# Kernel tuning notes

Measured on AMD Instinct MI355X. Metric: run time of the kernel, lower is better.

The kernel has to match this reference:

```python
import jax, jax.numpy as jnp
import numpy as np


def _bilinear2d(uv, table):
    """Bilinear lookup with wrap addressing; sigmoid non-linearity applied per
    corner (normalize=True in SpatialGrid2D), matching training-time forward.
    uv: (N,2) in [0,1); table: (U,V,L). Returns (N,L)."""
    U, V, _ = table.shape
    su = uv[:, 0] * U
    sv = uv[:, 1] * V
    u0 = jnp.floor(su)
    v0 = jnp.floor(sv)
    fu = (su - u0)[:, None]  # fractional weights, (N,1)
    fv = (sv - v0)[:, None]
    u0i = jnp.mod(u0.astype(jnp.int32), U)
    v0i = jnp.mod(v0.astype(jnp.int32), V)
    u1i = jnp.mod(u0i + 1, U)
    v1i = jnp.mod(v0i + 1, V)
    t00 = jax.nn.sigmoid(table[u0i, v0i])
    t10 = jax.nn.sigmoid(table[u1i, v0i])
    t01 = jax.nn.sigmoid(table[u0i, v1i])
    t11 = jax.nn.sigmoid(table[u1i, v1i])
    return (t00 * (1 - fu) + t10 * fu) * (1 - fv) + (t01 * (1 - fu) + t11 * fu) * fv


def setup_inputs() -> dict:
    key = jax.random.key(0)
    k1, k2, k3 = jax.random.split(key, 3)
    N = 2048 * 2048  # query points (one per pixel)
    RES = 520        # grid0 resolution from nativeResolution=4096, compression=6
    x = jax.random.uniform(k1, (N, 2), dtype=jnp.float32)
    grid1_table = jax.random.normal(k2, (RES * 4, RES * 4, 2), dtype=jnp.float32)
    grid0_table = jax.random.normal(k3, (RES, RES, 3), dtype=jnp.float32)
    return {"x": x, "grid1_table": grid1_table, "grid0_table": grid0_table}


def reference(x, grid1_table, grid0_table):
    # forward: grid0(grid1(x)) -- chained bilinear indirection lookups
    key = _bilinear2d(x, grid1_table)   # (N,2) indirected uv coords in (0,1)
    return _bilinear2d(key, grid0_table)  # (N,3) decoded RGB
```

## Files before the change

### kernel.cpp

```cpp
#include <hip/hip_runtime.h>
#include <math.h>


typedef float f32x2 __attribute__((ext_vector_type(2)));
typedef float f32x4 __attribute__((ext_vector_type(4)));

__device__ __forceinline__ float mul_rn_nocontract(float a, float b) {
    float r;
    asm("v_mul_f32 %0, %1, %2" : "=v"(r) : "v"(a), "v"(b));
    return r;
}

__device__ __forceinline__ float sigmoid_f64(float t) {
    double e = exp(-(double)t);
    return (float)(1.0 / (1.0 + e));
}

__device__ __forceinline__ float sigmoid_fast(float t) {
    return 1.0f / (1.0f + __expf(-t));
}

__global__ void __launch_bounds__(256) sigmoid_table_kernel(
    const float4* __restrict__ in, float4* __restrict__ out, int n4)
{
    int i = blockIdx.x * blockDim.x + threadIdx.x;
    if (i >= n4) return;
    float4 v = in[i];
    float4 r;
    r.x = sigmoid_f64(v.x);
    r.y = sigmoid_f64(v.y);
    r.z = sigmoid_f64(v.z);
    r.w = sigmoid_f64(v.w);
    out[i] = r;
}

__global__ void __launch_bounds__(256) pack_corners_kernel(
    const float* __restrict__ g1, float* __restrict__ pk, int U1)
{
    int c = blockIdx.x * blockDim.x + threadIdx.x;
    int ncells = U1 * U1;
    if (c >= ncells) return;
    int u = c / U1;
    int v = c - u * U1;
    int u1 = (u + 1 == U1) ? 0 : u + 1;
    int v1 = (v + 1 == U1) ? 0 : v + 1;
    const float2* g = reinterpret_cast<const float2*>(g1);
    float2 a = g[u * U1 + v];
    float2 b = g[u * U1 + v1];
    float2 d = g[u1 * U1 + v];
    float2 e = g[u1 * U1 + v1];
    float4 lo = make_float4(sigmoid_f64(a.x), sigmoid_f64(a.y),
                            sigmoid_f64(b.x), sigmoid_f64(b.y));
    float4 hi = make_float4(sigmoid_f64(d.x), sigmoid_f64(d.y),
                            sigmoid_f64(e.x), sigmoid_f64(e.y));
    float4* o = reinterpret_cast<float4*>(pk + (size_t)c * 8);
    o[0] = lo;
    o[1] = hi;
}

__global__ void __launch_bounds__(256) query_packed_kernel(
    const float* __restrict__ x,
    const float* __restrict__ pk,
    const float* __restrict__ s0,
    float* __restrict__ out,
    int N, int U1, int U0)
{
    int i = blockIdx.x * blockDim.x + threadIdx.x;
    if (i >= N) return;

    f32x2 uv = __builtin_nontemporal_load(
        reinterpret_cast<const f32x2*>(x) + i);

    float fU1 = (float)U1;
    float su = mul_rn_nocontract(uv.x, fU1);
    float sv = mul_rn_nocontract(uv.y, fU1);
    float u0f = floorf(su), v0f = floorf(sv);
    float fu = su - u0f;
    float fv = sv - v0f;
    int u0 = (int)u0f % U1; if (u0 < 0) u0 += U1;
    int v0 = (int)v0f % U1; if (v0 < 0) v0 += U1;

    const float4* cell = reinterpret_cast<const float4*>(pk)
                       + (size_t)(u0 * U1 + v0) * 2;
    float4 lo = cell[0];
    float4 hi = cell[1];

    float omfu = 1.0f - fu, omfv = 1.0f - fv;
    float kx = (lo.x * omfu + hi.x * fu) * omfv
             + (lo.z * omfu + hi.z * fu) * fv;
    float ky = (lo.y * omfu + hi.y * fu) * omfv
             + (lo.w * omfu + hi.w * fu) * fv;

    float fU0 = (float)U0;
    float su2 = mul_rn_nocontract(kx, fU0);
    float sv2 = mul_rn_nocontract(ky, fU0);
    float u0f2 = floorf(su2), v0f2 = floorf(sv2);
    float fu2 = su2 - u0f2, fv2 = sv2 - v0f2;
    int p0 = (int)u0f2 % U0; if (p0 < 0) p0 += U0;
    int q0 = (int)v0f2 % U0; if (q0 < 0) q0 += U0;
    int p1 = p0 + 1; if (p1 >= U0) p1 = 0;
    int q1 = q0 + 1; if (q1 >= U0) q1 = 0;
    int b00 = (p0 * U0 + q0) * 3, b10 = (p1 * U0 + q0) * 3;
    int b01 = (p0 * U0 + q1) * 3, b11 = (p1 * U0 + q1) * 3;
    float omfu2 = 1.0f - fu2, omfv2 = 1.0f - fv2;
    float r0 = (s0[b00+0] * omfu2 + s0[b10+0] * fu2) * omfv2
             + (s0[b01+0] * omfu2 + s0[b11+0] * fu2) * fv2;
    float r1 = (s0[b00+1] * omfu2 + s0[b10+1] * fu2) * omfv2
             + (s0[b01+1] * omfu2 + s0[b11+1] * fu2) * fv2;
    float r2 = (s0[b00+2] * omfu2 + s0[b10+2] * fu2) * omfv2
             + (s0[b01+2] * omfu2 + s0[b11+2] * fu2) * fv2;
    out[3*i+0] = r0; out[3*i+1] = r1; out[3*i+2] = r2;
}

__global__ void __launch_bounds__(256) query_kernel_unpadded(
    const float* __restrict__ x,
    const float* __restrict__ s1,
    const float* __restrict__ s0,
    float* __restrict__ out,
    int N, int U1, int U0)
{
    int i = blockIdx.x * blockDim.x + threadIdx.x;
    if (i >= N) return;
    float2 uv = reinterpret_cast<const float2*>(x)[i];
    float fU1 = (float)U1;
    float su = mul_rn_nocontract(uv.x, fU1);
    float sv = mul_rn_nocontract(uv.y, fU1);
    float u0f = floorf(su), v0f = floorf(sv);
    float fu = su - u0f, fv = sv - v0f;
    int u0 = (int)u0f % U1; if (u0 < 0) u0 += U1;
    int v0 = (int)v0f % U1; if (v0 < 0) v0 += U1;
    int u1 = u0 + 1; if (u1 >= U1) u1 = 0;
    int v1 = v0 + 1; if (v1 >= U1) v1 = 0;
    const float2* s1v = reinterpret_cast<const float2*>(s1);
    float2 t00 = s1v[u0 * U1 + v0];
    float2 t10 = s1v[u1 * U1 + v0];
    float2 t01 = s1v[u0 * U1 + v1];
    float2 t11 = s1v[u1 * U1 + v1];
    float omfu = 1.0f - fu, omfv = 1.0f - fv;
    float kx = (t00.x * omfu + t10.x * fu) * omfv + (t01.x * omfu + t11.x * fu) * fv;
    float ky = (t00.y * omfu + t10.y * fu) * omfv + (t01.y * omfu + t11.y * fu) * fv;
    float fU0 = (float)U0;
    float su2 = mul_rn_nocontract(kx, fU0);
    float sv2 = mul_rn_nocontract(ky, fU0);
    float u0f2 = floorf(su2), v0f2 = floorf(sv2);
    float fu2 = su2 - u0f2, fv2 = sv2 - v0f2;
    int p0 = (int)u0f2 % U0; if (p0 < 0) p0 += U0;
    int q0 = (int)v0f2 % U0; if (q0 < 0) q0 += U0;
    int p1 = p0 + 1; if (p1 >= U0) p1 = 0;
    int q1 = q0 + 1; if (q1 >= U0) q1 = 0;
    int b00 = (p0 * U0 + q0) * 3, b10 = (p1 * U0 + q0) * 3;
    int b01 = (p0 * U0 + q1) * 3, b11 = (p1 * U0 + q1) * 3;
    float omfu2 = 1.0f - fu2, omfv2 = 1.0f - fv2;
    float r0 = (s0[b00+0] * omfu2 + s0[b10+0] * fu2) * omfv2
             + (s0[b01+0] * omfu2 + s0[b11+0] * fu2) * fv2;
    float r1 = (s0[b00+1] * omfu2 + s0[b10+1] * fu2) * omfv2
             + (s0[b01+1] * omfu2 + s0[b11+1] * fu2) * fv2;
    float r2 = (s0[b00+2] * omfu2 + s0[b10+2] * fu2) * omfv2
             + (s0[b01+2] * omfu2 + s0[b11+2] * fu2) * fv2;
    out[3*i+0] = r0; out[3*i+1] = r1; out[3*i+2] = r2;
}

__global__ void __launch_bounds__(256) query_kernel_fallback(
    const float* __restrict__ x,
    const float* __restrict__ g1,
    const float* __restrict__ g0,
    float* __restrict__ out,
    int N, int U1, int U0)
{
    int i = blockIdx.x * blockDim.x + threadIdx.x;
    if (i >= N) return;
    float2 uv = reinterpret_cast<const float2*>(x)[i];
    float fU1 = (float)U1;
    float su = mul_rn_nocontract(uv.x, fU1);
    float sv = mul_rn_nocontract(uv.y, fU1);
    float u0f = floorf(su), v0f = floorf(sv);
    float fu = su - u0f, fv = sv - v0f;
    int u0 = (int)u0f % U1; if (u0 < 0) u0 += U1;
    int v0 = (int)v0f % U1; if (v0 < 0) v0 += U1;
    int u1 = u0 + 1; if (u1 >= U1) u1 = 0;
    int v1 = v0 + 1; if (v1 >= U1) v1 = 0;
    const float2* g1v = reinterpret_cast<const float2*>(g1);
    float2 t00 = g1v[u0 * U1 + v0];
    float2 t10 = g1v[u1 * U1 + v0];
    float2 t01 = g1v[u0 * U1 + v1];
    float2 t11 = g1v[u1 * U1 + v1];
    float a00x = sigmoid_f64(t00.x), a00y = sigmoid_f64(t00.y);
    float a10x = sigmoid_f64(t10.x), a10y = sigmoid_f64(t10.y);
    float a01x = sigmoid_f64(t01.x), a01y = sigmoid_f64(t01.y);
    float a11x = sigmoid_f64(t11.x), a11y = sigmoid_f64(t11.y);
    float omfu = 1.0f - fu, omfv = 1.0f - fv;
    float kx = (a00x * omfu + a10x * fu) * omfv + (a01x * omfu + a11x * fu) * fv;
    float ky = (a00y * omfu + a10y * fu) * omfv + (a01y * omfu + a11y * fu) * fv;
    float fU0 = (float)U0;
    float su2 = mul_rn_nocontract(kx, fU0);
    float sv2 = mul_rn_nocontract(ky, fU0);
    float u0f2 = floorf(su2), v0f2 = floorf(sv2);
    float fu2 = su2 - u0f2, fv2 = sv2 - v0f2;
    int p0 = (int)u0f2 % U0; if (p0 < 0) p0 += U0;
    int q0 = (int)v0f2 % U0; if (q0 < 0) q0 += U0;
    int p1 = p0 + 1; if (p1 >= U0) p1 = 0;
    int q1 = q0 + 1; if (q1 >= U0) q1 = 0;
    int b00 = (p0 * U0 + q0) * 3, b10 = (p1 * U0 + q0) * 3;
    int b01 = (p0 * U0 + q1) * 3, b11 = (p1 * U0 + q1) * 3;
    float omfu2 = 1.0f - fu2, omfv2 = 1.0f - fv2;
    float r0 = (sigmoid_fast(g0[b00+0]) * omfu2 + sigmoid_fast(g0[b10+0]) * fu2) * omfv2
             + (sigmoid_fast(g0[b01+0]) * omfu2 + sigmoid_fast(g0[b11+0]) * fu2) * fv2;
    float r1 = (sigmoid_fast(g0[b00+1]) * omfu2 + sigmoid_fast(g0[b10+1]) * fu2) * omfv2
             + (sigmoid_fast(g0[b01+1]) * omfu2 + sigmoid_fast(g0[b11+1]) * fu2) * fv2;
    float r2 = (sigmoid_fast(g0[b00+2]) * omfu2 + sigmoid_fast(g0[b10+2]) * fu2) * omfv2
             + (sigmoid_fast(g0[b01+2]) * omfu2 + sigmoid_fast(g0[b11+2]) * fu2) * fv2;
    out[3*i+0] = r0; out[3*i+1] = r1; out[3*i+2] = r2;
}

extern "C" void kernel_launch(void* const* d_in, const int* in_sizes, int n_in,
                              void* d_out, int out_size, void* d_ws, size_t ws_size,
                              hipStream_t stream) {
    const float* x  = (const float*)d_in[0];
    const float* g1 = (const float*)d_in[1];
    const float* g0 = (const float*)d_in[2];
    float* out = (float*)d_out;

    int N = in_sizes[0] / 2;
    long long n1 = in_sizes[1];
    long long n0 = in_sizes[2];
    int U1 = (int)(sqrt((double)(n1 / 2)) + 0.5);
    int U0 = (int)(sqrt((double)(n0 / 3)) + 0.5);
    long long ncells1 = (long long)U1 * U1;

    int block = 256;
    size_t need_packed = ((size_t)ncells1 * 8 + (size_t)n0) * sizeof(float);
    size_t need_plain  = ((size_t)n1 + (size_t)n0) * sizeof(float);

    if (ws_size >= need_packed && (n0 % 4) == 0) {
        float* pk = (float*)d_ws;
        float* s0 = pk + ncells1 * 8;
        int n0_4 = (int)(n0 / 4);
        pack_corners_kernel<<<(int)((ncells1 + block - 1) / block), block, 0, stream>>>(
            g1, pk, U1);
        sigmoid_table_kernel<<<(n0_4 + block - 1) / block, block, 0, stream>>>(
            (const float4*)g0, (float4*)s0, n0_4);
        query_packed_kernel<<<(N + block - 1) / block, block, 0, stream>>>(
            x, pk, s0, out, N, U1, U0);
    } else if (ws_size >= need_plain && (n1 % 4) == 0 && (n0 % 4) == 0) {
        float* s1 = (float*)d_ws;
        float* s0 = s1 + n1;
        int n1_4 = (int)(n1 / 4), n0_4 = (int)(n0 / 4);
        sigmoid_table_kernel<<<(n1_4 + block - 1) / block, block, 0, stream>>>(
            (const float4*)g1, (float4*)s1, n1_4);
        sigmoid_table_kernel<<<(n0_4 + block - 1) / block, block, 0, stream>>>(
            (const float4*)g0, (float4*)s0, n0_4);
        query_kernel_unpadded<<<(N + block - 1) / block, block, 0, stream>>>(
            x, s1, s0, out, N, U1, U0);
    } else {
        query_kernel_fallback<<<(N + block - 1) / block, block, 0, stream>>>(
            x, g1, g0, out, N, U1, U0);
    }
}
```

Measured before the change: 263.8 us.

## Tile corner-packing through LDS and process two query points per thread

The corner-packing kernel now loads a 17x17 tile of the grid1 table into shared memory and computes each sigmoid once per tile, instead of four f64 sigmoids per cell. This removes the redundant double-precision exp work and the repeated gathers. The query kernel handles two points per thread with a vectorized 16-byte input load and nontemporal vector output stores, which exposes more memory-level parallelism. In exchange it raises register pressure and adds an odd-N tail path.

```diff
diff --git a/kernel.cpp b/kernel.cpp
--- a/kernel.cpp
+++ b/kernel.cpp
@@ -34,82 +34,124 @@
     out[i] = r;
 }
 
-__global__ void __launch_bounds__(256) pack_corners_kernel(
-    const float* __restrict__ g1, float* __restrict__ pk, int U1)
-{
-    int c = blockIdx.x * blockDim.x + threadIdx.x;
-    int ncells = U1 * U1;
-    if (c >= ncells) return;
-    int u = c / U1;
-    int v = c - u * U1;
-    int u1 = (u + 1 == U1) ? 0 : u + 1;
-    int v1 = (v + 1 == U1) ? 0 : v + 1;
+__global__ void __launch_bounds__(256) pack_tiled_kernel(
+    const float* __restrict__ g1, float* __restrict__ pk,
+    int U1, int tiles_per_row)
+{
+    __shared__ float sx[17][17];
+    __shared__ float sy[17][17];
+
+    int tile = blockIdx.x;
+    int tu = tile / tiles_per_row;
+    int tv = tile - tu * tiles_per_row;
+    int ubase = tu * 16, vbase = tv * 16;
+
     const float2* g = reinterpret_cast<const float2*>(g1);
-    float2 a = g[u * U1 + v];
-    float2 b = g[u * U1 + v1];
-    float2 d = g[u1 * U1 + v];
-    float2 e = g[u1 * U1 + v1];
-    float4 lo = make_float4(sigmoid_f64(a.x), sigmoid_f64(a.y),
-                            sigmoid_f64(b.x), sigmoid_f64(b.y));
-    float4 hi = make_float4(sigmoid_f64(d.x), sigmoid_f64(d.y),
-                            sigmoid_f64(e.x), sigmoid_f64(e.y));
-    float4* o = reinterpret_cast<float4*>(pk + (size_t)c * 8);
-    o[0] = lo;
-    o[1] = hi;
-}
-
-__global__ void __launch_bounds__(256) query_packed_kernel(
+    for (int idx = threadIdx.x; idx < 17 * 17; idx += 256) {
+        int du = idx / 17, dv = idx - du * 17;
+        int u = ubase + du; if (u >= U1) u -= U1;
+        int v = vbase + dv; if (v >= U1) v -= U1;
+        float2 t = g[(size_t)u * U1 + v];
+        sx[du][dv] = sigmoid_f64(t.x);
+        sy[du][dv] = sigmoid_f64(t.y);
+    }
+    __syncthreads();
+
+    int lu = threadIdx.x >> 4, lv = threadIdx.x & 15;
+    int u = ubase + lu, v = vbase + lv;
+    if (u >= U1 || v >= U1) return;
+    f32x4 lo = {sx[lu][lv],     sy[lu][lv],     sx[lu][lv + 1],     sy[lu][lv + 1]};
+    f32x4 hi = {sx[lu + 1][lv], sy[lu + 1][lv], sx[lu + 1][lv + 1], sy[lu + 1][lv + 1]};
+    f32x4* o = reinterpret_cast<f32x4*>(pk + ((size_t)u * U1 + v) * 8);
+    __builtin_nontemporal_store(lo, o);
+    __builtin_nontemporal_store(hi, o + 1);
+}
+
+__global__ void __launch_bounds__(256) query2_packed_kernel(
     const float* __restrict__ x,
     const float* __restrict__ pk,
     const float* __restrict__ s0,
     float* __restrict__ out,
     int N, int U1, int U0)
 {
-    int i = blockIdx.x * blockDim.x + threadIdx.x;
-    if (i >= N) return;
-
-    f32x2 uv = __builtin_nontemporal_load(
-        reinterpret_cast<const f32x2*>(x) + i);
+    int t = blockIdx.x * blockDim.x + threadIdx.x;
+    int i0 = t * 2;
+    if (i0 >= N) return;
+    bool two = (i0 + 1 < N);
+
+    f32x4 xv = __builtin_nontemporal_load(reinterpret_cast<const f32x4*>(x) + t);
+    if (!two) { xv.z = xv.x; xv.w = xv.y; }
+
+    float ux[2] = {xv.x, xv.z};
+    float uy[2] = {xv.y, xv.w};
 
     float fU1 = (float)U1;
-    float su = mul_rn_nocontract(uv.x, fU1);
-    float sv = mul_rn_nocontract(uv.y, fU1);
-    float u0f = floorf(su), v0f = floorf(sv);
-    float fu = su - u0f;
-    float fv = sv - v0f;
-    int u0 = (int)u0f % U1; if (u0 < 0) u0 += U1;
-    int v0 = (int)v0f % U1; if (v0 < 0) v0 += U1;
-
-    const float4* cell = reinterpret_cast<const float4*>(pk)
-                       + (size_t)(u0 * U1 + v0) * 2;
-    float4 lo = cell[0];
-    float4 hi = cell[1];
-
-    float omfu = 1.0f - fu, omfv = 1.0f - fv;
-    float kx = (lo.x * omfu + hi.x * fu) * omfv
-             + (lo.z * omfu + hi.z * fu) * fv;
-    float ky = (lo.y * omfu + hi.y * fu) * omfv
-             + (lo.w * omfu + hi.w * fu) * fv;
+    float fu[2], fv[2];
+    size_t cidx[2];
+#pragma unroll
+    for (int p = 0; p < 2; ++p) {
+        float su = mul_rn_nocontract(ux[p], fU1);
+        float sv = mul_rn_nocontract(uy[p], fU1);
+        float u0f = floorf(su), v0f = floorf(sv);
+        fu[p] = su - u0f;
+        fv[p] = sv - v0f;
+        int u0 = (int)u0f % U1; if (u0 < 0) u0 += U1;
+        int v0 = (int)v0f % U1; if (v0 < 0) v0 += U1;
+        cidx[p] = (size_t)(u0 * U1 + v0) * 2;
+    }
+
+    const float4* pkv = reinterpret_cast<const float4*>(pk);
+    float4 lo[2], hi[2];
+#pragma unroll
+    for (int p = 0; p < 2; ++p) {
+        lo[p] = pkv[cidx[p]];
+        hi[p] = pkv[cidx[p] + 1];
+    }
+
+    float kx[2], ky[2];
+#pragma unroll
+    for (int p = 0; p < 2; ++p) {
+        float omfu = 1.0f - fu[p], omfv = 1.0f - fv[p];
+        kx[p] = (lo[p].x * omfu + hi[p].x * fu[p]) * omfv
+              + (lo[p].z * omfu + hi[p].z * fu[p]) * fv[p];
+        ky[p] = (lo[p].y * omfu + hi[p].y * fu[p]) * omfv
+              + (lo[p].w * omfu + hi[p].w * fu[p]) * fv[p];
+    }
 
     float fU0 = (float)U0;
-    float su2 = mul_rn_nocontract(kx, fU0);
-    float sv2 = mul_rn_nocontract(ky, fU0);
-    float u0f2 = floorf(su2), v0f2 = floorf(sv2);
-    float fu2 = su2 - u0f2, fv2 = sv2 - v0f2;
-    int p0 = (int)u0f2 % U0; if (p0 < 0) p0 += U0;
-    int q0 = (int)v0f2 % U0; if (q0 < 0) q0 += U0;
-    int p1 = p0 + 1; if (p1 >= U0) p1 = 0;
-    int q1 = q0 + 1; if (q1 >= U0) q1 = 0;
-    int b00 = (p0 * U0 + q0) * 3, b10 = (p1 * U0 + q0) * 3;
-    int b01 = (p0 * U0 + q1) * 3, b11 = (p1 * U0 + q1) * 3;
-    float omfu2 = 1.0f - fu2, omfv2 = 1.0f - fv2;
-    float r0 = (s0[b00+0] * omfu2 + s0[b10+0] * fu2) * omfv2
-             + (s0[b01+0] * omfu2 + s0[b11+0] * fu2) * fv2;
-    float r1 = (s0[b00+1] * omfu2 + s0[b10+1] * fu2) * omfv2
-             + (s0[b01+1] * omfu2 + s0[b11+1] * fu2) * fv2;
-    float r2 = (s0[b00+2] * omfu2 + s0[b10+2] * fu2) * omfv2
-             + (s0[b01+2] * omfu2 + s0[b11+2] * fu2) * fv2;
-    out[3*i+0] = r0; out[3*i+1] = r1; out[3*i+2] = r2;
+    float res[6];
+#pragma unroll
+    for (int p = 0; p < 2; ++p) {
+        float su2 = mul_rn_nocontract(kx[p], fU0);
+        float sv2 = mul_rn_nocontract(ky[p], fU0);
+        float u0f2 = floorf(su2), v0f2 = floorf(sv2);
+        float fu2 = su2 - u0f2, fv2 = sv2 - v0f2;
+        int p0 = (int)u0f2 % U0; if (p0 < 0) p0 += U0;
+        int q0 = (int)v0f2 % U0; if (q0 < 0) q0 += U0;
+        int p1 = p0 + 1; if (p1 >= U0) p1 = 0;
+        int q1 = q0 + 1; if (q1 >= U0) q1 = 0;
+        int b00 = (p0 * U0 + q0) * 3, b10 = (p1 * U0 + q0) * 3;
+        int b01 = (p0 * U0 + q1) * 3, b11 = (p1 * U0 + q1) * 3;
+        float omfu2 = 1.0f - fu2, omfv2 = 1.0f - fv2;
+        res[3*p+0] = (s0[b00+0] * omfu2 + s0[b10+0] * fu2) * omfv2
+                   + (s0[b01+0] * omfu2 + s0[b11+0] * fu2) * fv2;
+        res[3*p+1] = (s0[b00+1] * omfu2 + s0[b10+1] * fu2) * omfv2
+                   + (s0[b01+1] * omfu2 + s0[b11+1] * fu2) * fv2;
+        res[3*p+2] = (s0[b00+2] * omfu2 + s0[b10+2] * fu2) * omfv2
+                   + (s0[b01+2] * omfu2 + s0[b11+2] * fu2) * fv2;
+    }
+
+    float* op = out + (size_t)i0 * 3;
+    if (two) {
+        f32x2 o0 = {res[0], res[1]};
+        f32x2 o1 = {res[2], res[3]};
+        f32x2 o2 = {res[4], res[5]};
+        __builtin_nontemporal_store(o0, reinterpret_cast<f32x2*>(op));
+        __builtin_nontemporal_store(o1, reinterpret_cast<f32x2*>(op + 2));
+        __builtin_nontemporal_store(o2, reinterpret_cast<f32x2*>(op + 4));
+    } else {
+        op[0] = res[0]; op[1] = res[1]; op[2] = res[2];
+    }
 }
 
 __global__ void __launch_bounds__(256) query_kernel_unpadded(
@@ -235,11 +277,13 @@
         float* pk = (float*)d_ws;
         float* s0 = pk + ncells1 * 8;
         int n0_4 = (int)(n0 / 4);
-        pack_corners_kernel<<<(int)((ncells1 + block - 1) / block), block, 0, stream>>>(
-            g1, pk, U1);
+        int tiles_per_row = (U1 + 15) / 16;
+        int ntiles = tiles_per_row * tiles_per_row;
+        pack_tiled_kernel<<<ntiles, block, 0, stream>>>(g1, pk, U1, tiles_per_row);
         sigmoid_table_kernel<<<(n0_4 + block - 1) / block, block, 0, stream>>>(
             (const float4*)g0, (float4*)s0, n0_4);
-        query_packed_kernel<<<(N + block - 1) / block, block, 0, stream>>>(
+        int nthreads = (N + 1) / 2;
+        query2_packed_kernel<<<(nthreads + block - 1) / block, block, 0, stream>>>(
             x, pk, s0, out, N, U1, U0);
     } else if (ws_size >= need_plain && (n1 % 4) == 0 && (n0 % 4) == 0) {
         float* s1 = (float*)d_ws;
```

New measurement: 288.3 us. +9.3%, slower.

## Tile grid1 corner packing via shared memory and store grid0 sigmoid in SoA

Applied to the files above, without the earlier changes.

The grid1 corner-packing kernel now stages a 17x17 halo tile of sigmoid values in shared memory. Each table entry's float64 sigmoid is computed about once instead of four times, and reads are coalesced. The grid0 sigmoid table is stored as three planar arrays with padding, so the query kernel fetches adjacent q0/q1 pairs with 8-byte loads, one per row per channel. This replaces twelve scalar gathers, at the cost of a wrap-around branch and extra workspace.

```diff
diff --git a/kernel.cpp b/kernel.cpp
--- a/kernel.cpp
+++ b/kernel.cpp
@@ -20,48 +20,65 @@
     return 1.0f / (1.0f + __expf(-t));
 }
 
-__global__ void __launch_bounds__(256) sigmoid_table_kernel(
-    const float4* __restrict__ in, float4* __restrict__ out, int n4)
-{
-    int i = blockIdx.x * blockDim.x + threadIdx.x;
-    if (i >= n4) return;
-    float4 v = in[i];
-    float4 r;
-    r.x = sigmoid_f64(v.x);
-    r.y = sigmoid_f64(v.y);
-    r.z = sigmoid_f64(v.z);
-    r.w = sigmoid_f64(v.w);
-    out[i] = r;
-}
-
-__global__ void __launch_bounds__(256) pack_corners_kernel(
-    const float* __restrict__ g1, float* __restrict__ pk, int U1)
-{
-    int c = blockIdx.x * blockDim.x + threadIdx.x;
-    int ncells = U1 * U1;
-    if (c >= ncells) return;
-    int u = c / U1;
-    int v = c - u * U1;
-    int u1 = (u + 1 == U1) ? 0 : u + 1;
-    int v1 = (v + 1 == U1) ? 0 : v + 1;
+__device__ __forceinline__ f32x2 load2(const float* p) {
+    f32x2 v;
+    __builtin_memcpy(&v, p, 8);
+    return v;
+}
+
+__global__ void __launch_bounds__(256) pack_tiled_kernel(
+    const float* __restrict__ g1, float* __restrict__ pk,
+    int U1, int tiles_per_row)
+{
+    __shared__ float sx[17][17];
+    __shared__ float sy[17][17];
+
+    int tile = blockIdx.x;
+    int tu = tile / tiles_per_row;
+    int tv = tile - tu * tiles_per_row;
+    int ubase = tu * 16, vbase = tv * 16;
+
     const float2* g = reinterpret_cast<const float2*>(g1);
-    float2 a = g[u * U1 + v];
-    float2 b = g[u * U1 + v1];
-    float2 d = g[u1 * U1 + v];
-    float2 e = g[u1 * U1 + v1];
-    float4 lo = make_float4(sigmoid_f64(a.x), sigmoid_f64(a.y),
-                            sigmoid_f64(b.x), sigmoid_f64(b.y));
-    float4 hi = make_float4(sigmoid_f64(d.x), sigmoid_f64(d.y),
-                            sigmoid_f64(e.x), sigmoid_f64(e.y));
-    float4* o = reinterpret_cast<float4*>(pk + (size_t)c * 8);
+    for (int idx = threadIdx.x; idx < 17 * 17; idx += 256) {
+        int du = idx / 17, dv = idx - du * 17;
+        int u = ubase + du; if (u >= U1) u -= U1;
+        int v = vbase + dv; if (v >= U1) v -= U1;
+        float2 t = g[(size_t)u * U1 + v];
+        sx[du][dv] = sigmoid_f64(t.x);
+        sy[du][dv] = sigmoid_f64(t.y);
+    }
+    __syncthreads();
+
+    int lu = threadIdx.x >> 4, lv = threadIdx.x & 15;
+    int u = ubase + lu, v = vbase + lv;
+    if (u >= U1 || v >= U1) return;
+    float4 lo = make_float4(sx[lu][lv],     sy[lu][lv],
+                            sx[lu][lv + 1], sy[lu][lv + 1]);
+    float4 hi = make_float4(sx[lu + 1][lv],     sy[lu + 1][lv],
+                            sx[lu + 1][lv + 1], sy[lu + 1][lv + 1]);
+    float4* o = reinterpret_cast<float4*>(pk + ((size_t)u * U1 + v) * 8);
     o[0] = lo;
     o[1] = hi;
 }
 
-__global__ void __launch_bounds__(256) query_packed_kernel(
+__global__ void __launch_bounds__(256) sigmoid_soa_kernel(
+    const float* __restrict__ g0,
+    float* __restrict__ pr, float* __restrict__ pg, float* __restrict__ pb,
+    int ncells)
+{
+    int j = blockIdx.x * blockDim.x + threadIdx.x;
+    if (j >= ncells) return;
+    pr[j] = sigmoid_f64(g0[3 * j + 0]);
+    pg[j] = sigmoid_f64(g0[3 * j + 1]);
+    pb[j] = sigmoid_f64(g0[3 * j + 2]);
+}
+
+__global__ void __launch_bounds__(256) query_soa_kernel(
     const float* __restrict__ x,
     const float* __restrict__ pk,
-    const float* __restrict__ s0,
+    const float* __restrict__ pr,
+    const float* __restrict__ pg,
+    const float* __restrict__ pb,
     float* __restrict__ out,
     int N, int U1, int U0)
 {
@@ -99,17 +116,31 @@
     int p0 = (int)u0f2 % U0; if (p0 < 0) p0 += U0;
     int q0 = (int)v0f2 % U0; if (q0 < 0) q0 += U0;
     int p1 = p0 + 1; if (p1 >= U0) p1 = 0;
-    int q1 = q0 + 1; if (q1 >= U0) q1 = 0;
-    int b00 = (p0 * U0 + q0) * 3, b10 = (p1 * U0 + q0) * 3;
-    int b01 = (p0 * U0 + q1) * 3, b11 = (p1 * U0 + q1) * 3;
+    bool qwrap = (q0 == U0 - 1);
+
+    int rowA = p0 * U0 + q0;
+    int rowB = p1 * U0 + q0;
+    f32x2 ra = load2(pr + rowA), rb = load2(pr + rowB);
+    f32x2 ga = load2(pg + rowA), gb = load2(pg + rowB);
+    f32x2 ba = load2(pb + rowA), bb = load2(pb + rowB);
+    if (qwrap) {
+        int wA = p0 * U0, wB = p1 * U0;
+        ra.y = pr[wA]; rb.y = pr[wB];
+        ga.y = pg[wA]; gb.y = pg[wB];
+        ba.y = pb[wA]; bb.y = pb[wB];
+    }
+
     float omfu2 = 1.0f - fu2, omfv2 = 1.0f - fv2;
-    float r0 = (s0[b00+0] * omfu2 + s0[b10+0] * fu2) * omfv2
-             + (s0[b01+0] * omfu2 + s0[b11+0] * fu2) * fv2;
-    float r1 = (s0[b00+1] * omfu2 + s0[b10+1] * fu2) * omfv2
-             + (s0[b01+1] * omfu2 + s0[b11+1] * fu2) * fv2;
-    float r2 = (s0[b00+2] * omfu2 + s0[b10+2] * fu2) * omfv2
-             + (s0[b01+2] * omfu2 + s0[b11+2] * fu2) * fv2;
-    out[3*i+0] = r0; out[3*i+1] = r1; out[3*i+2] = r2;
+    float r0 = (ra.x * omfu2 + rb.x * fu2) * omfv2
+             + (ra.y * omfu2 + rb.y * fu2) * fv2;
+    float r1 = (ga.x * omfu2 + gb.x * fu2) * omfv2
+             + (ga.y * omfu2 + gb.y * fu2) * fv2;
+    float r2 = (ba.x * omfu2 + bb.x * fu2) * omfv2
+             + (ba.y * omfu2 + bb.y * fu2) * fv2;
+
+    out[3 * i + 0] = r0;
+    out[3 * i + 1] = r1;
+    out[3 * i + 2] = r2;
 }
 
 __global__ void __launch_bounds__(256) query_kernel_unpadded(
@@ -158,6 +189,20 @@
     float r2 = (s0[b00+2] * omfu2 + s0[b10+2] * fu2) * omfv2
              + (s0[b01+2] * omfu2 + s0[b11+2] * fu2) * fv2;
     out[3*i+0] = r0; out[3*i+1] = r1; out[3*i+2] = r2;
+}
+
+__global__ void __launch_bounds__(256) sigmoid_table_kernel(
+    const float4* __restrict__ in, float4* __restrict__ out, int n4)
+{
+    int i = blockIdx.x * blockDim.x + threadIdx.x;
+    if (i >= n4) return;
+    float4 v = in[i];
+    float4 r;
+    r.x = sigmoid_f64(v.x);
+    r.y = sigmoid_f64(v.y);
+    r.z = sigmoid_f64(v.z);
+    r.w = sigmoid_f64(v.w);
+    out[i] = r;
 }
 
 __global__ void __launch_bounds__(256) query_kernel_fallback(
@@ -226,21 +271,25 @@
     int U1 = (int)(sqrt((double)(n1 / 2)) + 0.5);
     int U0 = (int)(sqrt((double)(n0 / 3)) + 0.5);
     long long ncells1 = (long long)U1 * U1;
+    long long ncells0 = (long long)U0 * U0;
+    long long pstride = ncells0 + 16;
 
     int block = 256;
-    size_t need_packed = ((size_t)ncells1 * 8 + (size_t)n0) * sizeof(float);
-    size_t need_plain  = ((size_t)n1 + (size_t)n0) * sizeof(float);
-
-    if (ws_size >= need_packed && (n0 % 4) == 0) {
+    size_t need_soa   = ((size_t)ncells1 * 8 + 3 * (size_t)pstride) * sizeof(float);
+    size_t need_plain = ((size_t)n1 + (size_t)n0) * sizeof(float);
+
+    if (ws_size >= need_soa) {
         float* pk = (float*)d_ws;
-        float* s0 = pk + ncells1 * 8;
-        int n0_4 = (int)(n0 / 4);
-        pack_corners_kernel<<<(int)((ncells1 + block - 1) / block), block, 0, stream>>>(
-            g1, pk, U1);
-        sigmoid_table_kernel<<<(n0_4 + block - 1) / block, block, 0, stream>>>(
-            (const float4*)g0, (float4*)s0, n0_4);
-        query_packed_kernel<<<(N + block - 1) / block, block, 0, stream>>>(
-            x, pk, s0, out, N, U1, U0);
+        float* pr = pk + ncells1 * 8;
+        float* pg = pr + pstride;
+        float* pb = pg + pstride;
+        int tiles_per_row = (U1 + 15) / 16;
+        int ntiles = tiles_per_row * tiles_per_row;
+        pack_tiled_kernel<<<ntiles, block, 0, stream>>>(g1, pk, U1, tiles_per_row);
+        sigmoid_soa_kernel<<<(int)((ncells0 + block - 1) / block), block, 0, stream>>>(
+            g0, pr, pg, pb, (int)ncells0);
+        query_soa_kernel<<<(N + block - 1) / block, block, 0, stream>>>(
+            x, pk, pr, pg, pb, out, N, U1, U0);
     } else if (ws_size >= need_plain && (n1 % 4) == 0 && (n0 % 4) == 0) {
         float* s1 = (float*)d_ws;
         float* s0 = s1 + n1;
```

Result: slower. 289.6 us (+9.8%).

## Tile corner packing through shared memory and use float exp sigmoid

Applied to the files above, without the earlier changes.

Replaces the per-cell corner-packing kernel with a 16x16 tiled version. Each tile loads a 17x17 halo of the grid1 table into shared memory and evaluates the sigmoid once per texel rather than four times per cell. The double-precision exp sigmoid is also replaced by a float expf followed by a double reciprocal, which cuts FP64 transcendental cost. The trade-offs are a small numeric difference from the previous sigmoid and an extra block synchronisation.

```diff
diff --git a/kernel.cpp b/kernel.cpp
--- a/kernel.cpp
+++ b/kernel.cpp
@@ -11,13 +11,44 @@
     return r;
 }
 
-__device__ __forceinline__ float sigmoid_f64(float t) {
-    double e = exp(-(double)t);
-    return (float)(1.0 / (1.0 + e));
-}
-
-__device__ __forceinline__ float sigmoid_fast(float t) {
-    return 1.0f / (1.0f + __expf(-t));
+__device__ __forceinline__ float sigmoid_ref(float t) {
+    float e = expf(-t);
+    return (float)(1.0 / (1.0 + (double)e));
+}
+
+__global__ void __launch_bounds__(256) pack_tiled_kernel(
+    const float* __restrict__ g1, float* __restrict__ pk,
+    int U1, int tiles_per_row)
+{
+    __shared__ float sx[17][17];
+    __shared__ float sy[17][17];
+
+    int tile = blockIdx.x;
+    int tu = tile / tiles_per_row;
+    int tv = tile - tu * tiles_per_row;
+    int ubase = tu * 16, vbase = tv * 16;
+
+    const float2* g = reinterpret_cast<const float2*>(g1);
+    for (int idx = threadIdx.x; idx < 17 * 17; idx += 256) {
+        int du = idx / 17, dv = idx - du * 17;
+        int u = ubase + du; if (u >= U1) u -= U1;
+        int v = vbase + dv; if (v >= U1) v -= U1;
+        float2 t = g[(size_t)u * U1 + v];
+        sx[du][dv] = sigmoid_ref(t.x);
+        sy[du][dv] = sigmoid_ref(t.y);
+    }
+    __syncthreads();
+
+    int lu = threadIdx.x >> 4, lv = threadIdx.x & 15;
+    int u = ubase + lu, v = vbase + lv;
+    if (u >= U1 || v >= U1) return;
+    float4 lo = make_float4(sx[lu][lv],     sy[lu][lv],
+                            sx[lu][lv + 1], sy[lu][lv + 1]);
+    float4 hi = make_float4(sx[lu + 1][lv],     sy[lu + 1][lv],
+                            sx[lu + 1][lv + 1], sy[lu + 1][lv + 1]);
+    float4* o = reinterpret_cast<float4*>(pk + ((size_t)u * U1 + v) * 8);
+    o[0] = lo;
+    o[1] = hi;
 }
 
 __global__ void __launch_bounds__(256) sigmoid_table_kernel(
@@ -27,35 +58,11 @@
     if (i >= n4) return;
     float4 v = in[i];
     float4 r;
-    r.x = sigmoid_f64(v.x);
-    r.y = sigmoid_f64(v.y);
-    r.z = sigmoid_f64(v.z);
-    r.w = sigmoid_f64(v.w);
+    r.x = sigmoid_ref(v.x);
+    r.y = sigmoid_ref(v.y);
+    r.z = sigmoid_ref(v.z);
+    r.w = sigmoid_ref(v.w);
     out[i] = r;
-}
-
-__global__ void __launch_bounds__(256) pack_corners_kernel(
-    const float* __restrict__ g1, float* __restrict__ pk, int U1)
-{
-    int c = blockIdx.x * blockDim.x + threadIdx.x;
-    int ncells = U1 * U1;
-    if (c >= ncells) return;
-    int u = c / U1;
-    int v = c - u * U1;
-    int u1 = (u + 1 == U1) ? 0 : u + 1;
-    int v1 = (v + 1 == U1) ? 0 : v + 1;
-    const float2* g = reinterpret_cast<const float2*>(g1);
-    float2 a = g[u * U1 + v];
-    float2 b = g[u * U1 + v1];
-    float2 d = g[u1 * U1 + v];
-    float2 e = g[u1 * U1 + v1];
-    float4 lo = make_float4(sigmoid_f64(a.x), sigmoid_f64(a.y),
-                            sigmoid_f64(b.x), sigmoid_f64(b.y));
-    float4 hi = make_float4(sigmoid_f64(d.x), sigmoid_f64(d.y),
-                            sigmoid_f64(e.x), sigmoid_f64(e.y));
-    float4* o = reinterpret_cast<float4*>(pk + (size_t)c * 8);
-    o[0] = lo;
-    o[1] = hi;
 }
 
 __global__ void __launch_bounds__(256) query_packed_kernel(
@@ -184,10 +191,10 @@
     float2 t10 = g1v[u1 * U1 + v0];
     float2 t01 = g1v[u0 * U1 + v1];
     float2 t11 = g1v[u1 * U1 + v1];
-    float a00x = sigmoid_f64(t00.x), a00y = sigmoid_f64(t00.y);
-    float a10x = sigmoid_f64(t10.x), a10y = sigmoid_f64(t10.y);
-    float a01x = sigmoid_f64(t01.x), a01y = sigmoid_f64(t01.y);
-    float a11x = sigmoid_f64(t11.x), a11y = sigmoid_f64(t11.y);
+    float a00x = sigmoid_ref(t00.x), a00y = sigmoid_ref(t00.y);
+    float a10x = sigmoid_ref(t10.x), a10y = sigmoid_ref(t10.y);
+    float a01x = sigmoid_ref(t01.x), a01y = sigmoid_ref(t01.y);
+    float a11x = sigmoid_ref(t11.x), a11y = sigmoid_ref(t11.y);
     float omfu = 1.0f - fu, omfv = 1.0f - fv;
     float kx = (a00x * omfu + a10x * fu) * omfv + (a01x * omfu + a11x * fu) * fv;
     float ky = (a00y * omfu + a10y * fu) * omfv + (a01y * omfu + a11y * fu) * fv;
@@ -203,12 +210,12 @@
     int b00 = (p0 * U0 + q0) * 3, b10 = (p1 * U0 + q0) * 3;
     int b01 = (p0 * U0 + q1) * 3, b11 = (p1 * U0 + q1) * 3;
     float omfu2 = 1.0f - fu2, omfv2 = 1.0f - fv2;
-    float r0 = (sigmoid_fast(g0[b00+0]) * omfu2 + sigmoid_fast(g0[b10+0]) * fu2) * omfv2
-             + (sigmoid_fast(g0[b01+0]) * omfu2 + sigmoid_fast(g0[b11+0]) * fu2) * fv2;
-    float r1 = (sigmoid_fast(g0[b00+1]) * omfu2 + sigmoid_fast(g0[b10+1]) * fu2) * omfv2
-             + (sigmoid_fast(g0[b01+1]) * omfu2 + sigmoid_fast(g0[b11+1]) * fu2) * fv2;
-    float r2 = (sigmoid_fast(g0[b00+2]) * omfu2 + sigmoid_fast(g0[b10+2]) * fu2) * omfv2
-             + (sigmoid_fast(g0[b01+2]) * omfu2 + sigmoid_fast(g0[b11+2]) * fu2) * fv2;
+    float r0 = (sigmoid_ref(g0[b00+0]) * omfu2 + sigmoid_ref(g0[b10+0]) * fu2) * omfv2
+             + (sigmoid_ref(g0[b01+0]) * omfu2 + sigmoid_ref(g0[b11+0]) * fu2) * fv2;
+    float r1 = (sigmoid_ref(g0[b00+1]) * omfu2 + sigmoid_ref(g0[b10+1]) * fu2) * omfv2
+             + (sigmoid_ref(g0[b01+1]) * omfu2 + sigmoid_ref(g0[b11+1]) * fu2) * fv2;
+    float r2 = (sigmoid_ref(g0[b00+2]) * omfu2 + sigmoid_ref(g0[b10+2]) * fu2) * omfv2
+             + (sigmoid_ref(g0[b01+2]) * omfu2 + sigmoid_ref(g0[b11+2]) * fu2) * fv2;
     out[3*i+0] = r0; out[3*i+1] = r1; out[3*i+2] = r2;
 }
 
@@ -235,8 +242,9 @@
         float* pk = (float*)d_ws;
         float* s0 = pk + ncells1 * 8;
         int n0_4 = (int)(n0 / 4);
-        pack_corners_kernel<<<(int)((ncells1 + block - 1) / block), block, 0, stream>>>(
-            g1, pk, U1);
+        int tiles_per_row = (U1 + 15) / 16;
+        int ntiles = tiles_per_row * tiles_per_row;
+        pack_tiled_kernel<<<ntiles, block, 0, stream>>>(g1, pk, U1, tiles_per_row);
         sigmoid_table_kernel<<<(n0_4 + block - 1) / block, block, 0, stream>>>(
             (const float4*)g0, (float4*)s0, n0_4);
         query_packed_kernel<<<(N + block - 1) / block, block, 0, stream>>>(
```

Result: faster. 256.1 us (-2.9%).
